# Optimization experiments

Hardware: AMD Instinct MI355X
Metric: run time of the kernel (lower is better)

## Reference

```python
import jax, jax.numpy as jnp
import numpy as np

N_EMBD = 1024  # C in forward; scale is C**-0.5 (full embed dim, per source)


def setup_inputs() -> dict:
    key = jax.random.key(0)
    k1, k2, k3, k4 = jax.random.split(key, 4)
    B, T, C, H = 4, 4096, N_EMBD, 64
    x = jax.random.normal(k1, (B, T, C), dtype=jnp.float32)
    # weights stored as [in, out] = [n_embd, head_size]
    Wq = jax.random.normal(k2, (C, H), dtype=jnp.float32) * (C ** -0.5)
    Wk = jax.random.normal(k3, (C, H), dtype=jnp.float32) * (C ** -0.5)
    Wv = jax.random.normal(k4, (C, H), dtype=jnp.float32) * (C ** -0.5)
    return {"x": x, "Wq": Wq, "Wk": Wk, "Wv": Wv}


def reference(x, Wq, Wk, Wv):
    # x: [B, T, C]; projections to head_size H
    C = x.shape[-1]
    q = jnp.einsum('btc,ch->bth', x, Wq)  # [B,T,H]
    k = jnp.einsum('btc,ch->bth', x, Wk)  # [B,T,H]
    v = jnp.einsum('btc,ch->bth', x, Wv)  # [B,T,H]
    # scores scaled by C**-0.5 (full embed dim, matching original module)
    wei = jnp.einsum('bth,bsh->bts', q, k) * (C ** -0.5)  # [B,T,T]
    wei = jax.nn.softmax(wei, axis=-1)  # dropout p=0 -> identity
    out = jnp.einsum('bts,bsh->bth', wei, v)  # [B,T,H]
    return out
```

## Files before the change

### kernel.cpp

```cpp
#include <hip/hip_runtime.h>
#include <hip/hip_bf16.h>


#define BB 4
#define TT 4096
#define CC 1024
#define HH 64

typedef __attribute__((ext_vector_type(8))) short bf16x8;
typedef __attribute__((ext_vector_type(4))) float f32x4;

#if __has_builtin(__builtin_amdgcn_exp2f)
#define EXP2(x) __builtin_amdgcn_exp2f(x)
#else
#define EXP2(x) exp2f(x)
#endif

__device__ __forceinline__ short f2bf(float f) {
  union { float f; unsigned u; } v; v.f = f;
  unsigned r = v.u + 0x7fffu + ((v.u >> 16) & 1u);
  return (short)(r >> 16);
}

__device__ __forceinline__ short p2bf(float f) {
  union { float f; unsigned u; } v; v.f = f;
  return (short)((v.u + 0x8000u) >> 16);
}

__global__ void wtf_kernel(const float* __restrict__ Wq, const float* __restrict__ Wk,
                           const float* __restrict__ Wv, short* __restrict__ WtF) {
  int idx = blockIdx.x * 256 + threadIdx.x;
  int lane = idx & 63, ks = (idx >> 6) & 31, nf = idx >> 11;
  int l15 = lane & 15, lg = lane >> 4;
  int n = nf * 16 + l15;
  const float* W = (n < HH) ? Wq : ((n < 2 * HH) ? Wk : Wv);
  float sc = (n < HH) ? (0.03125f * 1.44269504f) : 1.0f;
  int k0 = ks * 32 + lg * 8, h = n & (HH - 1);
  bf16x8 r;
#pragma unroll
  for (int j = 0; j < 8; ++j) r[j] = f2bf(W[(k0 + j) * HH + h] * sc);
  *(bf16x8*)(WtF + (size_t)idx * 8) = r;
}

__launch_bounds__(256, 4)
__global__ void proj_kernel(const float* __restrict__ x, const short* __restrict__ WtF,
                            short* __restrict__ qo, short* __restrict__ kFo,
                            short* __restrict__ vFo) {
  __shared__ __align__(16) short xs[16 * 1024];
  int t = threadIdx.x;
  int row0 = blockIdx.x * 16;

  {
    int r = t >> 4, kc = t & 15;
    const float4* xr4 = (const float4*)(x + (size_t)(row0 + r) * CC) + kc * 2;
#pragma unroll
    for (int i = 0; i < 8; ++i) {
      float4 a = xr4[i * 32], b2 = xr4[i * 32 + 1];
      bf16x8 w;
      w[0] = f2bf(a.x);  w[1] = f2bf(a.y);  w[2] = f2bf(a.z);  w[3] = f2bf(a.w);
      w[4] = f2bf(b2.x); w[5] = f2bf(b2.y); w[6] = f2bf(b2.z); w[7] = f2bf(b2.w);
      int c = kc + i * 16;
      int S = (c * 256 + r * 16) ^ ((c & 7) << 4);
      *(bf16x8*)((char*)xs + S) = w;
    }
  }
  __syncthreads();

  int wave = t >> 6, lane = t & 63;
  int l15 = lane & 15, lg = lane >> 4;
  int nf0 = wave * 3;
  const short* wp = WtF + ((size_t)nf0 * 32 * 64 + (size_t)lane) * 8;
  const char* xsb = (const char*)xs;

  f32x4 acc[3];
#pragma unroll
  for (int j = 0; j < 3; ++j) acc[j] = (f32x4){0.f, 0.f, 0.f, 0.f};

  bf16x8 wA[3], wB[3];
#pragma unroll
  for (int j = 0; j < 3; ++j) wA[j] = *(const bf16x8*)(wp + (size_t)j * 32 * 512);

#pragma unroll
  for (int ks = 0; ks < 32; ks += 2) {
#pragma unroll
    for (int j = 0; j < 3; ++j)
      wB[j] = *(const bf16x8*)(wp + ((size_t)j * 32 + ks + 1) * 512);
    bf16x8 a0 = *(const bf16x8*)(xsb + ks * 1024 +
                   ((lane * 16) ^ ((((ks * 4) + lg) & 7) << 4)));
#pragma unroll
    for (int j = 0; j < 3; ++j)
      acc[j] = __builtin_amdgcn_mfma_f32_16x16x32_bf16(a0, wA[j], acc[j], 0, 0, 0);
    if (ks + 2 < 32) {
#pragma unroll
      for (int j = 0; j < 3; ++j)
        wA[j] = *(const bf16x8*)(wp + ((size_t)j * 32 + ks + 2) * 512);
    }
    bf16x8 a1 = *(const bf16x8*)(xsb + (ks + 1) * 1024 +
                   ((lane * 16) ^ (((((ks + 1) * 4) + lg) & 7) << 4)));
#pragma unroll
    for (int j = 0; j < 3; ++j)
      acc[j] = __builtin_amdgcn_mfma_f32_16x16x32_bf16(a1, wB[j], acc[j], 0, 0, 0);
  }

  int b  = row0 >> 12;
  int kt = (row0 & 4095) >> 6;
  int cf = (row0 >> 4) & 3;
  short* ksl = xs;
  short* vsl = xs + 1152;

  __syncthreads();

#pragma unroll
  for (int j = 0; j < 3; ++j) {
    int nf = nf0 + j;
    int h = (nf & 3) * 16 + l15;
    if (nf < 4) {
#pragma unroll
      for (int reg = 0; reg < 4; ++reg)
        qo[(size_t)(row0 + lg * 4 + reg) * HH + h] = f2bf(acc[j][reg]);
    } else if (nf < 8) {
#pragma unroll
      for (int reg = 0; reg < 4; ++reg)
        ksl[(lg * 4 + reg) * 72 + h] = f2bf(acc[j][reg]);
    } else {
      short4 s4;
      s4.x = f2bf(acc[j][0]); s4.y = f2bf(acc[j][1]);
      s4.z = f2bf(acc[j][2]); s4.w = f2bf(acc[j][3]);
      *(short4*)(vsl + h * 24 + lg * 4) = s4;
    }
  }
  __syncthreads();

  size_t tileoff = ((size_t)b * 64 + kt) * 4096;
  if (t < 128) {
    int ks2 = t >> 6, ln = t & 63;
    int l15o = ln & 15, lgo = ln >> 4;
    bf16x8 r = *(const bf16x8*)(ksl + l15o * 72 + ks2 * 32 + lgo * 8);
    *(bf16x8*)(kFo + tileoff + (size_t)(cf * 2 + ks2) * 512 + ln * 8) = r;
  } else if (t < 256) {
    int t2 = t - 128;
    int hf = t2 >> 5, lgl = (t2 >> 4) & 1, l15o = t2 & 15;
    bf16x8 r = *(const bf16x8*)(vsl + (hf * 16 + l15o) * 24 + lgl * 8);
    int lnout = (2 * (cf & 1) + lgl) * 16 + l15o;
    *(bf16x8*)(vFo + tileoff + (size_t)(hf * 2 + (cf >> 1)) * 512 + lnout * 8) = r;
  }
}

__launch_bounds__(512, 4)
__global__ void attnW_kernel(const short* __restrict__ q, const short* __restrict__ kF,
                             const short* __restrict__ vF, float* __restrict__ out) {
  __shared__ __align__(16) short ps[8][2560];
  __shared__ __align__(16) float macc[32][68];
  __shared__ float lL[32];
  int wave = threadIdx.x >> 6, lane = threadIdx.x & 63;
  int l15 = lane & 15, lg = lane >> 4;
  int low3 = blockIdx.x & 7;
  int b  = low3 >> 1;
  int qt = ((blockIdx.x >> 3) << 1) | (low3 & 1);
  int brow0 = qt * 32;

  const short* qb = q + ((size_t)b * TT + brow0 + l15) * HH;
  bf16x8 qa[2][2];
#pragma unroll
  for (int g = 0; g < 2; ++g) {
    qa[g][0] = *(const bf16x8*)(qb + g * 16 * HH + lg * 8);
    qa[g][1] = *(const bf16x8*)(qb + g * 16 * HH + 32 + lg * 8);
  }

  bf16x8 ones;
#pragma unroll
  for (int j = 0; j < 8; ++j) ones[j] = (short)0x3F80;

  const short* kfb = kF + (size_t)b * 262144 + (size_t)lane * 8;
  const short* vfb = vF + (size_t)b * 262144 + (size_t)lane * 8;

  f32x4 acc[2][4], accl[2];
#pragma unroll
  for (int g = 0; g < 2; ++g) {
#pragma unroll
    for (int i = 0; i < 4; ++i) acc[g][i] = (f32x4){0.f, 0.f, 0.f, 0.f};
    accl[g] = (f32x4){0.f, 0.f, 0.f, 0.f};
  }

  char* psw = (char*)&ps[wave][0];
  int pw = lg * 320 + ((l15 * 2) ^ ((lg >> 1) << 4));
  int pr = l15 * 80 + ((lg ^ (l15 >> 3)) << 4);

  for (int t = wave * 16; t < wave * 16 + 16; ++t) {
    const short* kp = kfb + (size_t)t * 2048;
    const short* vp = vfb + (size_t)(t >> 1) * 4096 + (size_t)(t & 1) * 512;
    bf16x8 kf[4], vf[4];
#pragma unroll
    for (int ld = 0; ld < 4; ++ld) kf[ld] = *(const bf16x8*)(kp + ld * 512);
#pragma unroll
    for (int hf = 0; hf < 4; ++hf) vf[hf] = *(const bf16x8*)(vp + hf * 1024);
#pragma unroll
    for (int g = 0; g < 2; ++g)
#pragma unroll
      for (int cf = 0; cf < 2; ++cf) {
        f32x4 t4 = (f32x4){0.f, 0.f, 0.f, 0.f};
        t4 = __builtin_amdgcn_mfma_f32_16x16x32_bf16(qa[g][0], kf[cf * 2], t4, 0, 0, 0);
        t4 = __builtin_amdgcn_mfma_f32_16x16x32_bf16(qa[g][1], kf[cf * 2 + 1], t4, 0, 0, 0);
#pragma unroll
        for (int reg = 0; reg < 4; ++reg) {
          float p = EXP2(t4[reg]);
          *(short*)(psw + (g * 1280 + pw + reg * 80 + cf * 32)) = p2bf(p);
        }
      }
    bf16x8 pa0 = *(const bf16x8*)(psw + pr);
    bf16x8 pa1 = *(const bf16x8*)(psw + 1280 + pr);
    __builtin_amdgcn_s_setprio(1);
#pragma unroll
    for (int hf = 0; hf < 4; ++hf) {
      acc[0][hf] = __builtin_amdgcn_mfma_f32_16x16x32_bf16(pa0, vf[hf], acc[0][hf], 0, 0, 0);
      acc[1][hf] = __builtin_amdgcn_mfma_f32_16x16x32_bf16(pa1, vf[hf], acc[1][hf], 0, 0, 0);
    }
    accl[0] = __builtin_amdgcn_mfma_f32_16x16x32_bf16(pa0, ones, accl[0], 0, 0, 0);
    accl[1] = __builtin_amdgcn_mfma_f32_16x16x32_bf16(pa1, ones, accl[1], 0, 0, 0);
    __builtin_amdgcn_s_setprio(0);
  }

#pragma unroll
  for (int ph = 0; ph < 8; ++ph) {
    if (wave == ph) {
#pragma unroll
      for (int g = 0; g < 2; ++g)
#pragma unroll
        for (int reg = 0; reg < 4; ++reg) {
          int row = g * 16 + lg * 4 + reg;
          if (ph == 0) {
#pragma unroll
            for (int hf = 0; hf < 4; ++hf)
              macc[row][hf * 16 + l15] = acc[g][hf][reg];
            if (l15 == 0) lL[row] = accl[g][reg];
          } else {
#pragma unroll
            for (int hf = 0; hf < 4; ++hf)
              macc[row][hf * 16 + l15] += acc[g][hf][reg];
            if (l15 == 0) lL[row] += accl[g][reg];
          }
        }
    }
    __syncthreads();
  }

  {
    int tt = threadIdx.x;
    int r = tt >> 4, c0 = (tt & 15) * 4;
    float linv = 1.0f / lL[r];
    float4 o;
    o.x = macc[r][c0 + 0] * linv; o.y = macc[r][c0 + 1] * linv;
    o.z = macc[r][c0 + 2] * linv; o.w = macc[r][c0 + 3] * linv;
    *(float4*)(out + ((size_t)b * TT + brow0 + r) * HH + c0) = o;
  }
}

extern "C" void kernel_launch(void* const* d_in, const int* in_sizes, int n_in,
                              void* d_out, int out_size, void* d_ws, size_t ws_size,
                              hipStream_t stream) {
  const float* x  = (const float*)d_in[0];
  const float* Wq = (const float*)d_in[1];
  const float* Wk = (const float*)d_in[2];
  const float* Wv = (const float*)d_in[3];
  float* out = (float*)d_out;

  char* ws = (char*)d_ws;
  short* WtF = (short*)ws;
  short* q   = (short*)(ws + 0x080000);
  short* kF  = (short*)(ws + 0x280000);
  short* vF  = (short*)(ws + 0x480000);

  hipLaunchKernelGGL(wtf_kernel,   dim3(96),   dim3(256), 0, stream, Wq, Wk, Wv, WtF);
  hipLaunchKernelGGL(proj_kernel,  dim3(1024), dim3(256), 0, stream, x, WtF, q, kF, vF);
  hipLaunchKernelGGL(attnW_kernel, dim3(512),  dim3(512), 0, stream, q, kF, vF, out);
}
```

Baseline: 64.42 us.

## Double rows per projection block and transpose QK MFMA for packed P stores

The projection kernel now handles 32 rows per block in two K-halves, so each weight fragment loaded from global memory feeds two MFMA row groups, and the grid is halved. In the attention kernel the QK^T MFMA operands are swapped so each lane holds a transposed score tile. The four exponentials can then be packed into two 32-bit bf16x2 LDS stores instead of four scalar short stores, using a new XOR swizzle. The cost is an extra barrier and LDS refill per block, fewer blocks in the projection, and RNE bf16 conversion of P where the old code rounded by adding 0x8000.

Result: slower. 72.01 us (+11.8%).

```diff
diff --git a/kernel.cpp b/kernel.cpp
--- a/kernel.cpp
+++ b/kernel.cpp
@@ -20,11 +20,6 @@
   union { float f; unsigned u; } v; v.f = f;
   unsigned r = v.u + 0x7fffu + ((v.u >> 16) & 1u);
   return (short)(r >> 16);
-}
-
-__device__ __forceinline__ short p2bf(float f) {
-  union { float f; unsigned u; } v; v.f = f;
-  return (short)((v.u + 0x8000u) >> 16);
 }
 
 __global__ void wtf_kernel(const float* __restrict__ Wq, const float* __restrict__ Wk,
@@ -48,101 +43,122 @@
                             short* __restrict__ vFo) {
   __shared__ __align__(16) short xs[16 * 1024];
   int t = threadIdx.x;
-  int row0 = blockIdx.x * 16;
-
-  {
-    int r = t >> 4, kc = t & 15;
-    const float4* xr4 = (const float4*)(x + (size_t)(row0 + r) * CC) + kc * 2;
-#pragma unroll
-    for (int i = 0; i < 8; ++i) {
-      float4 a = xr4[i * 32], b2 = xr4[i * 32 + 1];
-      bf16x8 w;
-      w[0] = f2bf(a.x);  w[1] = f2bf(a.y);  w[2] = f2bf(a.z);  w[3] = f2bf(a.w);
-      w[4] = f2bf(b2.x); w[5] = f2bf(b2.y); w[6] = f2bf(b2.z); w[7] = f2bf(b2.w);
-      int c = kc + i * 16;
-      int S = (c * 256 + r * 16) ^ ((c & 7) << 4);
-      *(bf16x8*)((char*)xs + S) = w;
-    }
-  }
-  __syncthreads();
-
+  int row0 = blockIdx.x * 32;
   int wave = t >> 6, lane = t & 63;
   int l15 = lane & 15, lg = lane >> 4;
   int nf0 = wave * 3;
   const short* wp = WtF + ((size_t)nf0 * 32 * 64 + (size_t)lane) * 8;
-  const char* xsb = (const char*)xs;
-
-  f32x4 acc[3];
-#pragma unroll
-  for (int j = 0; j < 3; ++j) acc[j] = (f32x4){0.f, 0.f, 0.f, 0.f};
-
-  bf16x8 wA[3], wB[3];
-#pragma unroll
-  for (int j = 0; j < 3; ++j) wA[j] = *(const bf16x8*)(wp + (size_t)j * 32 * 512);
-
-#pragma unroll
-  for (int ks = 0; ks < 32; ks += 2) {
+  char* xsb = (char*)xs;
+
+  f32x4 acc[2][3];
+#pragma unroll
+  for (int g = 0; g < 2; ++g)
+#pragma unroll
+    for (int j = 0; j < 3; ++j) acc[g][j] = (f32x4){0.f, 0.f, 0.f, 0.f};
+
+  for (int kh = 0; kh < 2; ++kh) {
+    if (kh) __syncthreads();
+    {
+      int r32 = t >> 3, kc = t & 7;
+      int g = r32 >> 4, r = r32 & 15;
+      const float4* xr4 = (const float4*)(x + (size_t)(row0 + r32) * CC + kh * 512) + kc * 2;
+#pragma unroll
+      for (int i = 0; i < 8; ++i) {
+        float4 a = xr4[i * 16], b2 = xr4[i * 16 + 1];
+        bf16x8 w;
+        w[0] = f2bf(a.x);  w[1] = f2bf(a.y);  w[2] = f2bf(a.z);  w[3] = f2bf(a.w);
+        w[4] = f2bf(b2.x); w[5] = f2bf(b2.y); w[6] = f2bf(b2.z); w[7] = f2bf(b2.w);
+        int c = kc + i * 8;
+        int S = g * 16384 + ((c * 256 + r * 16) ^ ((c & 7) << 4));
+        *(bf16x8*)(xsb + S) = w;
+      }
+    }
+    __syncthreads();
+
+    bf16x8 wA[3], wB[3];
 #pragma unroll
     for (int j = 0; j < 3; ++j)
-      wB[j] = *(const bf16x8*)(wp + ((size_t)j * 32 + ks + 1) * 512);
-    bf16x8 a0 = *(const bf16x8*)(xsb + ks * 1024 +
-                   ((lane * 16) ^ ((((ks * 4) + lg) & 7) << 4)));
-#pragma unroll
-    for (int j = 0; j < 3; ++j)
-      acc[j] = __builtin_amdgcn_mfma_f32_16x16x32_bf16(a0, wA[j], acc[j], 0, 0, 0);
-    if (ks + 2 < 32) {
+      wA[j] = *(const bf16x8*)(wp + ((size_t)j * 32 + kh * 16) * 512);
+
+#pragma unroll
+    for (int ksl = 0; ksl < 16; ksl += 2) {
+      int ks = kh * 16 + ksl;
 #pragma unroll
       for (int j = 0; j < 3; ++j)
-        wA[j] = *(const bf16x8*)(wp + ((size_t)j * 32 + ks + 2) * 512);
-    }
-    bf16x8 a1 = *(const bf16x8*)(xsb + (ks + 1) * 1024 +
-                   ((lane * 16) ^ (((((ks + 1) * 4) + lg) & 7) << 4)));
-#pragma unroll
-    for (int j = 0; j < 3; ++j)
-      acc[j] = __builtin_amdgcn_mfma_f32_16x16x32_bf16(a1, wB[j], acc[j], 0, 0, 0);
-  }
-
-  int b  = row0 >> 12;
-  int kt = (row0 & 4095) >> 6;
-  int cf = (row0 >> 4) & 3;
-  short* ksl = xs;
-  short* vsl = xs + 1152;
+        wB[j] = *(const bf16x8*)(wp + ((size_t)j * 32 + ks + 1) * 512);
+      int sw0 = (lane * 16) ^ ((((ksl * 4) + lg) & 7) << 4);
+      bf16x8 a0g0 = *(const bf16x8*)(xsb + ksl * 1024 + sw0);
+      bf16x8 a0g1 = *(const bf16x8*)(xsb + 16384 + ksl * 1024 + sw0);
+#pragma unroll
+      for (int j = 0; j < 3; ++j) {
+        acc[0][j] = __builtin_amdgcn_mfma_f32_16x16x32_bf16(a0g0, wA[j], acc[0][j], 0, 0, 0);
+        acc[1][j] = __builtin_amdgcn_mfma_f32_16x16x32_bf16(a0g1, wA[j], acc[1][j], 0, 0, 0);
+      }
+      if (ksl + 2 < 16) {
+#pragma unroll
+        for (int j = 0; j < 3; ++j)
+          wA[j] = *(const bf16x8*)(wp + ((size_t)j * 32 + ks + 2) * 512);
+      }
+      int sw1 = (lane * 16) ^ (((((ksl + 1) * 4) + lg) & 7) << 4);
+      bf16x8 a1g0 = *(const bf16x8*)(xsb + (ksl + 1) * 1024 + sw1);
+      bf16x8 a1g1 = *(const bf16x8*)(xsb + 16384 + (ksl + 1) * 1024 + sw1);
+#pragma unroll
+      for (int j = 0; j < 3; ++j) {
+        acc[0][j] = __builtin_amdgcn_mfma_f32_16x16x32_bf16(a1g0, wB[j], acc[0][j], 0, 0, 0);
+        acc[1][j] = __builtin_amdgcn_mfma_f32_16x16x32_bf16(a1g1, wB[j], acc[1][j], 0, 0, 0);
+      }
+    }
+  }
 
   __syncthreads();
-
-#pragma unroll
-  for (int j = 0; j < 3; ++j) {
-    int nf = nf0 + j;
-    int h = (nf & 3) * 16 + l15;
-    if (nf < 4) {
-#pragma unroll
-      for (int reg = 0; reg < 4; ++reg)
-        qo[(size_t)(row0 + lg * 4 + reg) * HH + h] = f2bf(acc[j][reg]);
-    } else if (nf < 8) {
-#pragma unroll
-      for (int reg = 0; reg < 4; ++reg)
-        ksl[(lg * 4 + reg) * 72 + h] = f2bf(acc[j][reg]);
-    } else {
-      short4 s4;
-      s4.x = f2bf(acc[j][0]); s4.y = f2bf(acc[j][1]);
-      s4.z = f2bf(acc[j][2]); s4.w = f2bf(acc[j][3]);
-      *(short4*)(vsl + h * 24 + lg * 4) = s4;
+#pragma unroll
+  for (int g = 0; g < 2; ++g) {
+    int row0g = row0 + g * 16;
+    short* kslg = xs + g * 1152;
+    short* vslg = xs + 2304 + g * 1536;
+#pragma unroll
+    for (int j = 0; j < 3; ++j) {
+      int nf = nf0 + j;
+      int h = (nf & 3) * 16 + l15;
+      if (nf < 4) {
+#pragma unroll
+        for (int reg = 0; reg < 4; ++reg)
+          qo[(size_t)(row0g + lg * 4 + reg) * HH + h] = f2bf(acc[g][j][reg]);
+      } else if (nf < 8) {
+#pragma unroll
+        for (int reg = 0; reg < 4; ++reg)
+          kslg[(lg * 4 + reg) * 72 + h] = f2bf(acc[g][j][reg]);
+      } else {
+        short4 s4;
+        s4.x = f2bf(acc[g][j][0]); s4.y = f2bf(acc[g][j][1]);
+        s4.z = f2bf(acc[g][j][2]); s4.w = f2bf(acc[g][j][3]);
+        *(short4*)(vslg + h * 24 + lg * 4) = s4;
+      }
     }
   }
   __syncthreads();
 
-  size_t tileoff = ((size_t)b * 64 + kt) * 4096;
-  if (t < 128) {
-    int ks2 = t >> 6, ln = t & 63;
-    int l15o = ln & 15, lgo = ln >> 4;
-    bf16x8 r = *(const bf16x8*)(ksl + l15o * 72 + ks2 * 32 + lgo * 8);
-    *(bf16x8*)(kFo + tileoff + (size_t)(cf * 2 + ks2) * 512 + ln * 8) = r;
-  } else if (t < 256) {
-    int t2 = t - 128;
-    int hf = t2 >> 5, lgl = (t2 >> 4) & 1, l15o = t2 & 15;
-    bf16x8 r = *(const bf16x8*)(vsl + (hf * 16 + l15o) * 24 + lgl * 8);
-    int lnout = (2 * (cf & 1) + lgl) * 16 + l15o;
-    *(bf16x8*)(vFo + tileoff + (size_t)(hf * 2 + (cf >> 1)) * 512 + lnout * 8) = r;
+#pragma unroll
+  for (int g = 0; g < 2; ++g) {
+    int row0g = row0 + g * 16;
+    int b = row0g >> 12;
+    int kt = (row0g & 4095) >> 6;
+    int cf = (row0g >> 4) & 3;
+    const short* kslg = xs + g * 1152;
+    const short* vslg = xs + 2304 + g * 1536;
+    size_t tileoff = ((size_t)b * 64 + kt) * 4096;
+    if (t < 128) {
+      int ks2 = t >> 6, ln = t & 63;
+      int l15o = ln & 15, lgo = ln >> 4;
+      bf16x8 r = *(const bf16x8*)(kslg + l15o * 72 + ks2 * 32 + lgo * 8);
+      *(bf16x8*)(kFo + tileoff + (size_t)(cf * 2 + ks2) * 512 + ln * 8) = r;
+    } else if (t < 256) {
+      int t2 = t - 128;
+      int hf = t2 >> 5, lgl = (t2 >> 4) & 1, l15o = t2 & 15;
+      bf16x8 r = *(const bf16x8*)(vslg + (hf * 16 + l15o) * 24 + lgl * 8);
+      int lnout = (2 * (cf & 1) + lgl) * 16 + l15o;
+      *(bf16x8*)(vFo + tileoff + (size_t)(hf * 2 + (cf >> 1)) * 512 + lnout * 8) = r;
+    }
   }
 }
 
@@ -183,8 +199,9 @@
   }
 
   char* psw = (char*)&ps[wave][0];
-  int pw = lg * 320 + ((l15 * 2) ^ ((lg >> 1) << 4));
-  int pr = l15 * 80 + ((lg ^ (l15 >> 3)) << 4);
+  int xorv = (l15 >> 3) << 4;
+  int pwbase = l15 * 80;
+  int pr = l15 * 80 + ((lg << 4) ^ xorv);
 
   for (int t = wave * 16; t < wave * 16 + 16; ++t) {
     const short* kp = kfb + (size_t)t * 2048;
@@ -199,13 +216,17 @@
 #pragma unroll
       for (int cf = 0; cf < 2; ++cf) {
         f32x4 t4 = (f32x4){0.f, 0.f, 0.f, 0.f};
-        t4 = __builtin_amdgcn_mfma_f32_16x16x32_bf16(qa[g][0], kf[cf * 2], t4, 0, 0, 0);
-        t4 = __builtin_amdgcn_mfma_f32_16x16x32_bf16(qa[g][1], kf[cf * 2 + 1], t4, 0, 0, 0);
-#pragma unroll
-        for (int reg = 0; reg < 4; ++reg) {
-          float p = EXP2(t4[reg]);
-          *(short*)(psw + (g * 1280 + pw + reg * 80 + cf * 32)) = p2bf(p);
-        }
+        t4 = __builtin_amdgcn_mfma_f32_16x16x32_bf16(kf[cf * 2], qa[g][0], t4, 0, 0, 0);
+        t4 = __builtin_amdgcn_mfma_f32_16x16x32_bf16(kf[cf * 2 + 1], qa[g][1], t4, 0, 0, 0);
+        float p0 = EXP2(t4[0]), p1 = EXP2(t4[1]);
+        float p2 = EXP2(t4[2]), p3 = EXP2(t4[3]);
+        __hip_bfloat162 w01 = __float22bfloat162_rn(make_float2(p0, p1));
+        __hip_bfloat162 w23 = __float22bfloat162_rn(make_float2(p2, p3));
+        int cb = (cf << 5) + (lg << 3);
+        *(unsigned*)(psw + g * 1280 + pwbase + ((cb) ^ xorv)) =
+            *reinterpret_cast<unsigned*>(&w01);
+        *(unsigned*)(psw + g * 1280 + pwbase + ((cb + 4) ^ xorv)) =
+            *reinterpret_cast<unsigned*>(&w23);
       }
     bf16x8 pa0 = *(const bf16x8*)(psw + pr);
     bf16x8 pa1 = *(const bf16x8*)(psw + 1280 + pr);
@@ -270,7 +291,7 @@
   short* kF  = (short*)(ws + 0x280000);
   short* vF  = (short*)(ws + 0x480000);
 
-  hipLaunchKernelGGL(wtf_kernel,   dim3(96),   dim3(256), 0, stream, Wq, Wk, Wv, WtF);
-  hipLaunchKernelGGL(proj_kernel,  dim3(1024), dim3(256), 0, stream, x, WtF, q, kF, vF);
-  hipLaunchKernelGGL(attnW_kernel, dim3(512),  dim3(512), 0, stream, q, kF, vF, out);
-}
+  hipLaunchKernelGGL(wtf_kernel,   dim3(96),  dim3(256), 0, stream, Wq, Wk, Wv, WtF);
+  hipLaunchKernelGGL(proj_kernel,  dim3(512), dim3(256), 0, stream, x, WtF, q, kF, vF);
+  hipLaunchKernelGGL(attnW_kernel, dim3(512), dim3(512), 0, stream, q, kF, vF, out);
+}
```
